# Optimization experiments

Hardware: AMD Instinct MI355X
Metric: run time of the kernel (lower is better)

## Reference

```python
import jax, jax.numpy as jnp
import numpy as np


def channel_linear(h, W, b):
    # h: (b, s, n_in, d_channels); W: (d, n_out, n_in); b: (d, n_out)
    out = jnp.einsum('bsic,coi->bsoc', h, W)
    return out + b.T[None, None]  # (b, s, n_out, d)


def setup_inputs() -> dict:
    d, s, bsz = 64, 64, 512
    lt, p = d * (d - 1) // 2, d * d
    key = jax.random.key(0)
    ks = jax.random.split(key, 12)
    inp = {
        'x': jax.random.normal(ks[0], (bsz, d), dtype=jnp.float32),
        'z': jax.random.normal(ks[1], (s, lt + p), dtype=jnp.float32),
    }
    widths = [d, 32, 32, 32, 1]
    for li, (ni, no) in enumerate(zip(widths[:-1], widths[1:])):
        inp[f'W{li}'] = jax.random.normal(ks[2 + 2 * li], (d, no, ni), dtype=jnp.float32) / np.sqrt(ni).astype(np.float32)
        inp[f'b{li}'] = jax.random.normal(ks[3 + 2 * li], (d, no), dtype=jnp.float32) * 0.01
    return inp


def reference(x, z, W0, b0, W1, b1, W2, b2, W3, b3):
    d = x.shape[1]
    s = z.shape[0]
    lt_width = d * (d - 1) // 2
    rows, cols = np.tril_indices(d, -1)  # matches torch.tril_indices(d, d, offset=-1)

    # get_z_adjacency_lt_p: strictly-lower-triangular matrix conjugated by z_p
    z_lt = jnp.zeros((s, d, d), dtype=z.dtype).at[:, rows, cols].set(z[:, :lt_width])
    z_p = z[:, -d * d:].reshape(s, d, d)
    # z_p^T @ z_lt @ z_p
    z_adj = jnp.einsum('sri,srt,stj->sij', z_p, z_lt, z_p)  # (s, d, d)

    # broadcast multiply: h[b,s,i,j] = A[s,i,j] * x[b,i]
    h = z_adj[None, :, :, :] * x[:, None, :, None]  # (b, s, d, d)

    h = jax.nn.relu(channel_linear(h, W0, b0))  # (b, s, 32, d)
    h = jax.nn.relu(channel_linear(h, W1, b1))
    h = jax.nn.relu(channel_linear(h, W2, b2))
    out = jnp.squeeze(channel_linear(h, W3, b3), axis=-2)  # (b, s, d)
    return (out, z_adj)
```

## Files before the change

kernel.cpp:

```cpp
#include <hip/hip_runtime.h>
#include <math.h>

#define D 64
#define S 64
#define BSZ 512
#define LTW 2016
#define ZROW 6112
#define OUT0_SIZE (BSZ * S * D)
#define ZADJ_OFF  OUT0_SIZE

typedef float    f32x4 __attribute__((ext_vector_type(4)));
typedef _Float16 f16x8 __attribute__((ext_vector_type(8)));
typedef _Float16 f16x2 __attribute__((ext_vector_type(2)));

union V8 { f16x8 v; f16x2 h2[4]; uint4 u; };

__device__ __forceinline__ f16x2 pkrtz(float a, float b) {
    return __builtin_bit_cast(f16x2, __builtin_amdgcn_cvt_pkrtz(a, b));
}

__global__ __launch_bounds__(256) void k_zadjprep(
    const float* __restrict__ z, float* __restrict__ zadj,
    float* __restrict__ zt,
    const float* __restrict__ x,
    const float* __restrict__ W0, const float* __restrict__ W1,
    const float* __restrict__ W2,
    uint4* __restrict__ w0f, uint4* __restrict__ w1f,
    uint4* __restrict__ w2f, uint4* __restrict__ xf) {
    __shared__ float zp[4096];
    __shared__ float zlt[4160];
    __shared__ float T[1280];
    const int blk = blockIdx.x;
    const int tid = threadIdx.x;

    if (blk < 256) {
        const int s = blk >> 2, jt = blk & 3;
        const float* zs = z + (size_t)s * ZROW;
#pragma unroll
        for (int rep = 0; rep < 16; ++rep) {
            int idx = tid + rep * 256;
            zp[idx] = zs[LTW + idx];
        }
        for (int idx = tid; idx < 4160; idx += 256) zlt[idx] = 0.0f;
        __syncthreads();
        for (int k = tid; k < LTW; k += 256) {
            float kf = (float)k;
            int r = (int)((1.0f + sqrtf(1.0f + 8.0f * kf)) * 0.5f);
            while (r * (r - 1) / 2 > k) --r;
            while ((r + 1) * r / 2 <= k) ++r;
            int t = k - r * (r - 1) / 2;
            zlt[r * 65 + t] = zs[k];
        }
        __syncthreads();
        const int rr = tid & 63, wj = (tid >> 6) * 4;
        {
            f32x4 acc = {0.0f, 0.0f, 0.0f, 0.0f};
            for (int t = 0; t < 64; ++t) {
                float zl = zlt[rr * 65 + t];
                f32x4 zpv = *(const f32x4*)&zp[t * 64 + jt * 16 + wj];
#pragma unroll
                for (int q = 0; q < 4; ++q) acc[q] = fmaf(zl, zpv[q], acc[q]);
            }
            *(f32x4*)&T[rr * 20 + wj] = acc;
        }
        __syncthreads();
        {
            const int i = rr;
            f32x4 acc = {0.0f, 0.0f, 0.0f, 0.0f};
            for (int r = 0; r < 64; ++r) {
                float zv = zp[r * 64 + i];
                f32x4 tv = *(const f32x4*)&T[r * 20 + wj];
#pragma unroll
                for (int q = 0; q < 4; ++q) acc[q] = fmaf(zv, tv[q], acc[q]);
            }
            *(f32x4*)&zadj[(size_t)s * 4096 + i * 64 + jt * 16 + wj] = acc;
            if (zt) {
#pragma unroll
                for (int q = 0; q < 4; ++q)
                    zt[(size_t)s * 4096 + (jt * 16 + wj + q) * 64 + i] = acc[q];
            }
        }
    } else {
        const int c = blk - 256;
        const int sl = tid >> 6, ln = tid & 63;
        const int q = ln >> 4, l15 = ln & 15;
        {
            int Mt = sl >> 1, ks = sl & 1;
            const float* src = W0 + c * 2048 + (Mt * 16 + l15) * 64 + ks * 32 + q * 8;
            V8 hv;
#pragma unroll
            for (int j = 0; j < 8; ++j) hv.v[j] = (_Float16)src[j];
            w0f[(size_t)(c * 4 + sl) * 64 + ln] = hv.u;
        }
        {
            const float* Wsrc = (sl < 2) ? W1 : W2;
            uint4* dstb = (sl < 2) ? w1f : w2f;
            int Mt = sl & 1;
            const float* srow = Wsrc + c * 1024 + (Mt * 16 + l15) * 32;
            V8 hv;
#pragma unroll
            for (int j = 0; j < 8; ++j) {
                int k = ((j >> 2) << 4) + q * 4 + (j & 3);
                hv.v[j] = (_Float16)srow[k];
            }
            dstb[(size_t)(c * 2 + Mt) * 64 + ln] = hv.u;
        }
        if (tid < 64) {
            int f = c * 64 + tid;
            int fln = f & 63, ks = (f >> 6) & 1, bt = f >> 7;
            int n = bt * 16 + (fln & 15), i0 = ks * 32 + (fln >> 4) * 8;
            const float* src = x + n * 64 + i0;
            V8 hv;
#pragma unroll
            for (int j = 0; j < 8; ++j) hv.v[j] = (_Float16)src[j];
            xf[f] = hv.u;
        }
    }
}

template <bool ZT>
__global__ __launch_bounds__(256, 4) void k_main_mfma(
    const uint4* __restrict__ xf, const uint4* __restrict__ w0f,
    const uint4* __restrict__ w1f, const uint4* __restrict__ w2f,
    const float* __restrict__ zadj, const float* __restrict__ zadjT,
    const float* __restrict__ B0, const float* __restrict__ B1,
    const float* __restrict__ B2, const float* __restrict__ W3,
    const float* __restrict__ B3, float* __restrict__ outT) {
    const int bh = blockIdx.x;
    const int c = blockIdx.y, sg = blockIdx.z;
    const int tid = threadIdx.x;
    const int wave = tid >> 6, lane = tid & 63;
    const int quad = lane >> 4;
    const int btbase = bh * 16 + wave * 4;

    V8 a0[2][2];
#pragma unroll
    for (int Mt = 0; Mt < 2; ++Mt)
#pragma unroll
        for (int ks = 0; ks < 2; ++ks)
            a0[Mt][ks].u = w0f[(size_t)(c * 4 + Mt * 2 + ks) * 64 + lane];
    V8 a1[2], a2[2];
#pragma unroll
    for (int Mt = 0; Mt < 2; ++Mt) {
        a1[Mt].u = w1f[(size_t)(c * 2 + Mt) * 64 + lane];
        a2[Mt].u = w2f[(size_t)(c * 2 + Mt) * 64 + lane];
    }
    f32x4 b0v[2], b1v[2], b2v[2], w3v[2];
#pragma unroll
    for (int Mt = 0; Mt < 2; ++Mt) {
        int off = c * 32 + Mt * 16 + quad * 4;
        b0v[Mt] = *(const f32x4*)(B0 + off);
        b1v[Mt] = *(const f32x4*)(B1 + off);
        b2v[Mt] = *(const f32x4*)(B2 + off);
        w3v[Mt] = *(const f32x4*)(W3 + off);
    }
    const float b3v = B3[c];

#pragma unroll 1
    for (int it = 0; it < 4; ++it) {
        const int s = sg * 4 + it;
        f16x2 zvh[2][4];
        if (ZT) {
            const f32x4* ztp = (const f32x4*)(zadjT + (size_t)s * 4096 + c * 64);
            f32x4 zq[4];
            zq[0] = ztp[quad * 2];
            zq[1] = ztp[quad * 2 + 1];
            zq[2] = ztp[8 + quad * 2];
            zq[3] = ztp[8 + quad * 2 + 1];
#pragma unroll
            for (int ks = 0; ks < 2; ++ks)
#pragma unroll
                for (int t = 0; t < 4; ++t) {
                    const f32x4& v = zq[ks * 2 + (t >> 1)];
                    zvh[ks][t] = pkrtz(v[(t & 1) * 2], v[(t & 1) * 2 + 1]);
                }
        } else {
#pragma unroll
            for (int ks = 0; ks < 2; ++ks) {
                const float* zp = zadj + (size_t)s * 4096 + (ks * 32 + quad * 8) * 64 + c;
                float zv[8];
#pragma unroll
                for (int j = 0; j < 8; ++j) zv[j] = zp[j * 64];
#pragma unroll
                for (int t = 0; t < 4; ++t)
                    zvh[ks][t] = pkrtz(zv[2 * t], zv[2 * t + 1]);
            }
        }
        V8 a0s[2][2];
#pragma unroll
        for (int Mt = 0; Mt < 2; ++Mt)
#pragma unroll
            for (int ks = 0; ks < 2; ++ks)
#pragma unroll
                for (int t = 0; t < 4; ++t)
                    a0s[Mt][ks].h2[t] = a0[Mt][ks].h2[t] * zvh[ks][t];

        float red[4];
#pragma unroll
        for (int Nt = 0; Nt < 4; ++Nt) {
            f32x4 acc0[2] = {b0v[0], b0v[1]};
#pragma unroll
            for (int ks = 0; ks < 2; ++ks) {
                V8 xv;
                xv.u = xf[(size_t)((btbase + Nt) * 2 + ks) * 64 + lane];
#pragma unroll
                for (int Mt = 0; Mt < 2; ++Mt)
                    acc0[Mt] = __builtin_amdgcn_mfma_f32_16x16x32_f16(
                        a0s[Mt][ks].v, xv.v, acc0[Mt], 0, 0, 0);
            }
            V8 bb;
            bb.h2[0] = pkrtz(fmaxf(acc0[0][0], 0.0f), fmaxf(acc0[0][1], 0.0f));
            bb.h2[1] = pkrtz(fmaxf(acc0[0][2], 0.0f), fmaxf(acc0[0][3], 0.0f));
            bb.h2[2] = pkrtz(fmaxf(acc0[1][0], 0.0f), fmaxf(acc0[1][1], 0.0f));
            bb.h2[3] = pkrtz(fmaxf(acc0[1][2], 0.0f), fmaxf(acc0[1][3], 0.0f));
            f32x4 acc1[2] = {b1v[0], b1v[1]};
#pragma unroll
            for (int Mt = 0; Mt < 2; ++Mt)
                acc1[Mt] = __builtin_amdgcn_mfma_f32_16x16x32_f16(
                    a1[Mt].v, bb.v, acc1[Mt], 0, 0, 0);
            V8 cc;
            cc.h2[0] = pkrtz(fmaxf(acc1[0][0], 0.0f), fmaxf(acc1[0][1], 0.0f));
            cc.h2[1] = pkrtz(fmaxf(acc1[0][2], 0.0f), fmaxf(acc1[0][3], 0.0f));
            cc.h2[2] = pkrtz(fmaxf(acc1[1][0], 0.0f), fmaxf(acc1[1][1], 0.0f));
            cc.h2[3] = pkrtz(fmaxf(acc1[1][2], 0.0f), fmaxf(acc1[1][3], 0.0f));
            f32x4 acc2[2] = {b2v[0], b2v[1]};
#pragma unroll
            for (int Mt = 0; Mt < 2; ++Mt)
                acc2[Mt] = __builtin_amdgcn_mfma_f32_16x16x32_f16(
                    a2[Mt].v, cc.v, acc2[Mt], 0, 0, 0);
            float p = 0.0f;
#pragma unroll
            for (int Mt = 0; Mt < 2; ++Mt)
#pragma unroll
                for (int r = 0; r < 4; ++r)
                    p = fmaf(w3v[Mt][r], fmaxf(acc2[Mt][r], 0.0f), p);
            p += __shfl_xor(p, 16, 64);
            p += __shfl_xor(p, 32, 64);
            red[Nt] = p;
        }
        float outv = (quad & 2) ? ((quad & 1) ? red[3] : red[2])
                                : ((quad & 1) ? red[1] : red[0]);
        outv += b3v;
        outT[((size_t)s * 64 + c) * 512 + bh * 256 + tid] = outv;
    }
}

__global__ __launch_bounds__(256, 3) void k_main_valu(
    const float* __restrict__ xsrc, const float* __restrict__ zadj,
    const float* __restrict__ W0, const float* __restrict__ B0,
    const float* __restrict__ W1, const float* __restrict__ B1,
    const float* __restrict__ W2, const float* __restrict__ B2,
    const float* __restrict__ W3, const float* __restrict__ B3,
    float* __restrict__ outp, int o_sS, int o_cS, int o_bS) {
    const int c = blockIdx.x;
    const int s = blockIdx.y;
    const int lane = threadIdx.x & 63;
    const int wave = threadIdx.x >> 6;

    const float* w0c = W0 + c * 2048;
    const float* w1c = W1 + c * 1024;
    const float* w2c = W2 + c * 1024;
    const float* w3c = W3 + c * 32;
    const float* b0c = B0 + c * 32;
    const float* b1c = B1 + c * 32;
    const float* b2c = B2 + c * 32;
    const float b3v = B3[c];
    const float* zc = zadj + s * 4096 + c;

#pragma unroll 1
    for (int bc = 0; bc < 2; ++bc) {
        const int b = wave * 128 + bc * 64 + lane;
        float h1[32], h2[32];
#pragma unroll
        for (int o = 0; o < 32; ++o) h1[o] = b0c[o];
#pragma unroll 8
        for (int i = 0; i < 64; ++i) {
            float hi = zc[i * 64] * xsrc[b * 64 + i];
#pragma unroll
            for (int o = 0; o < 32; ++o) h1[o] = fmaf(w0c[o * 64 + i], hi, h1[o]);
        }
#pragma unroll
        for (int o = 0; o < 32; ++o) { h1[o] = fmaxf(h1[o], 0.0f); h2[o] = b1c[o]; }
#pragma unroll 8
        for (int j = 0; j < 32; ++j) {
            float v = h1[j];
#pragma unroll
            for (int o = 0; o < 32; ++o) h2[o] = fmaf(w1c[o * 32 + j], v, h2[o]);
        }
#pragma unroll
        for (int o = 0; o < 32; ++o) { h2[o] = fmaxf(h2[o], 0.0f); h1[o] = b2c[o]; }
#pragma unroll 8
        for (int j = 0; j < 32; ++j) {
            float v = h2[j];
#pragma unroll
            for (int o = 0; o < 32; ++o) h1[o] = fmaf(w2c[o * 32 + j], v, h1[o]);
        }
        float a = b3v;
#pragma unroll
        for (int j = 0; j < 32; ++j) a = fmaf(w3c[j], fmaxf(h1[j], 0.0f), a);
        outp[s * o_sS + c * o_cS + b * o_bS] = a;
    }
}

__global__ __launch_bounds__(256) void k_outT(const float* __restrict__ outT,
                                              float* __restrict__ out) {
    __shared__ float tile[64][65];
    const int bt = blockIdx.x;
    const int s = blockIdx.y;
    const int tid = threadIdx.x;
    const int r0 = tid >> 6, q = tid & 63;
#pragma unroll
    for (int rep = 0; rep < 16; ++rep) {
        int crow = rep * 4 + r0;
        tile[crow][q] = outT[(s * 64 + crow) * 512 + bt * 64 + q];
    }
    __syncthreads();
#pragma unroll
    for (int rep = 0; rep < 16; ++rep) {
        int brow = rep * 4 + r0;
        out[(bt * 64 + brow) * 4096 + s * 64 + q] = tile[q][brow];
    }
}

extern "C" void kernel_launch(void* const* d_in, const int* in_sizes, int n_in,
                              void* d_out, int out_size, void* d_ws, size_t ws_size,
                              hipStream_t stream) {
    const float* x  = (const float*)d_in[0];
    const float* z  = (const float*)d_in[1];
    const float* W0 = (const float*)d_in[2];
    const float* B0 = (const float*)d_in[3];
    const float* W1 = (const float*)d_in[4];
    const float* B1 = (const float*)d_in[5];
    const float* W2 = (const float*)d_in[6];
    const float* B2 = (const float*)d_in[7];
    const float* W3 = (const float*)d_in[8];
    const float* B3 = (const float*)d_in[9];

    float* out  = (float*)d_out;
    float* zadj = out + ZADJ_OFF;

    const size_t OT_B  = (size_t)S * D * BSZ * sizeof(float);
    const size_t XF_B  = 4096 * 16;
    const size_t W0F_B = (size_t)64 * 4 * 64 * 16;
    const size_t W1F_B = (size_t)64 * 2 * 64 * 16;
    const size_t W2F_B = W1F_B;
    const size_t ZT_B  = (size_t)S * 4096 * sizeof(float);
    const size_t FRAG_END = OT_B + XF_B + W0F_B + W1F_B + W2F_B;
    const bool has_oT   = ws_size >= OT_B;
    const bool has_frag = ws_size >= FRAG_END;
    const bool has_zt   = ws_size >= FRAG_END + ZT_B;

    char* wsb = (char*)d_ws;
    float* outT  = (float*)wsb;
    uint4* xf    = (uint4*)(wsb + OT_B);
    uint4* w0f   = (uint4*)(wsb + OT_B + XF_B);
    uint4* w1f   = (uint4*)(wsb + OT_B + XF_B + W0F_B);
    uint4* w2f   = (uint4*)(wsb + OT_B + XF_B + W0F_B + W1F_B);
    float* zadjT = (float*)(wsb + FRAG_END);

    if (has_frag) {
        hipLaunchKernelGGL(k_zadjprep, dim3(320), dim3(256), 0, stream,
                           z, zadj, has_zt ? zadjT : (float*)nullptr,
                           x, W0, W1, W2, w0f, w1f, w2f, xf);
        if (has_zt)
            hipLaunchKernelGGL((k_main_mfma<true>), dim3(2, 64, 16), dim3(256),
                               0, stream, xf, w0f, w1f, w2f, zadj, zadjT,
                               B0, B1, B2, W3, B3, outT);
        else
            hipLaunchKernelGGL((k_main_mfma<false>), dim3(2, 64, 16), dim3(256),
                               0, stream, xf, w0f, w1f, w2f, zadj, zadjT,
                               B0, B1, B2, W3, B3, outT);
        hipLaunchKernelGGL(k_outT, dim3(8, S), dim3(256), 0, stream, outT, out);
    } else {
        hipLaunchKernelGGL(k_zadjprep, dim3(256), dim3(256), 0, stream,
                           z, zadj, (float*)nullptr, x, W0, W1, W2,
                           (uint4*)nullptr, (uint4*)nullptr, (uint4*)nullptr,
                           (uint4*)nullptr);
        float* op = has_oT ? outT : out;
        const int o_sS = has_oT ? (64 * 512) : 64;
        const int o_cS = has_oT ? 512 : 1;
        const int o_bS = has_oT ? 1 : 4096;
        hipLaunchKernelGGL(k_main_valu, dim3(D, S), dim3(256), 0, stream,
                           x, zadj, W0, B0, W1, B1, W2, B2, W3, B3,
                           op, o_sS, o_cS, o_bS);
        if (has_oT)
            hipLaunchKernelGGL(k_outT, dim3(8, S), dim3(256), 0, stream, outT, out);
    }
}
```

Measured before the change: 114.3 us.

## Hoist x fragments, apply packed fp16 ReLU, vectorize transpose, unroll prep loops

The x MFMA fragments are now loaded once into registers before the s-loop instead of being reloaded every iteration. ReLU is applied to the packed fp16 vectors after conversion rather than per float, and the launch bound drops to 3 waves per SIMD to leave room for the extra registers. The output transpose kernel switches to 16-byte vector global loads and stores, and the z-adjacency prep loops get unroll pragmas. The risks are lower occupancy, and that f16 ReLU after rounding-toward-zero conversion could differ slightly, though the results should be equivalent.

```diff
diff --git a/kernel.cpp b/kernel.cpp
--- a/kernel.cpp
+++ b/kernel.cpp
@@ -17,6 +17,16 @@
 
 __device__ __forceinline__ f16x2 pkrtz(float a, float b) {
     return __builtin_bit_cast(f16x2, __builtin_amdgcn_cvt_pkrtz(a, b));
+}
+__device__ __forceinline__ f16x8 relu8(f16x8 a) {
+#if __has_builtin(__builtin_elementwise_max)
+    return __builtin_elementwise_max(a, (f16x8)0);
+#else
+    f16x8 r;
+#pragma unroll
+    for (int i = 0; i < 8; ++i) r[i] = a[i] > (_Float16)0 ? a[i] : (_Float16)0;
+    return r;
+#endif
 }
 
 __global__ __launch_bounds__(256) void k_zadjprep(
@@ -55,6 +65,7 @@
         const int rr = tid & 63, wj = (tid >> 6) * 4;
         {
             f32x4 acc = {0.0f, 0.0f, 0.0f, 0.0f};
+#pragma unroll 8
             for (int t = 0; t < 64; ++t) {
                 float zl = zlt[rr * 65 + t];
                 f32x4 zpv = *(const f32x4*)&zp[t * 64 + jt * 16 + wj];
@@ -67,6 +78,7 @@
         {
             const int i = rr;
             f32x4 acc = {0.0f, 0.0f, 0.0f, 0.0f};
+#pragma unroll 8
             for (int r = 0; r < 64; ++r) {
                 float zv = zp[r * 64 + i];
                 f32x4 tv = *(const f32x4*)&T[r * 20 + wj];
@@ -119,7 +131,7 @@
 }
 
 template <bool ZT>
-__global__ __launch_bounds__(256, 4) void k_main_mfma(
+__global__ __launch_bounds__(256, 3) void k_main_mfma(
     const uint4* __restrict__ xf, const uint4* __restrict__ w0f,
     const uint4* __restrict__ w1f, const uint4* __restrict__ w2f,
     const float* __restrict__ zadj, const float* __restrict__ zadjT,
@@ -145,6 +157,12 @@
         a1[Mt].u = w1f[(size_t)(c * 2 + Mt) * 64 + lane];
         a2[Mt].u = w2f[(size_t)(c * 2 + Mt) * 64 + lane];
     }
+    V8 xv[4][2];
+#pragma unroll
+    for (int Nt = 0; Nt < 4; ++Nt)
+#pragma unroll
+        for (int ks = 0; ks < 2; ++ks)
+            xv[Nt][ks].u = xf[(size_t)((btbase + Nt) * 2 + ks) * 64 + lane];
     f32x4 b0v[2], b1v[2], b2v[2], w3v[2];
 #pragma unroll
     for (int Mt = 0; Mt < 2; ++Mt) {
@@ -200,29 +218,28 @@
         for (int Nt = 0; Nt < 4; ++Nt) {
             f32x4 acc0[2] = {b0v[0], b0v[1]};
 #pragma unroll
-            for (int ks = 0; ks < 2; ++ks) {
-                V8 xv;
-                xv.u = xf[(size_t)((btbase + Nt) * 2 + ks) * 64 + lane];
+            for (int ks = 0; ks < 2; ++ks)
 #pragma unroll
                 for (int Mt = 0; Mt < 2; ++Mt)
                     acc0[Mt] = __builtin_amdgcn_mfma_f32_16x16x32_f16(
-                        a0s[Mt][ks].v, xv.v, acc0[Mt], 0, 0, 0);
-            }
+                        a0s[Mt][ks].v, xv[Nt][ks].v, acc0[Mt], 0, 0, 0);
             V8 bb;
-            bb.h2[0] = pkrtz(fmaxf(acc0[0][0], 0.0f), fmaxf(acc0[0][1], 0.0f));
-            bb.h2[1] = pkrtz(fmaxf(acc0[0][2], 0.0f), fmaxf(acc0[0][3], 0.0f));
-            bb.h2[2] = pkrtz(fmaxf(acc0[1][0], 0.0f), fmaxf(acc0[1][1], 0.0f));
-            bb.h2[3] = pkrtz(fmaxf(acc0[1][2], 0.0f), fmaxf(acc0[1][3], 0.0f));
+            bb.h2[0] = pkrtz(acc0[0][0], acc0[0][1]);
+            bb.h2[1] = pkrtz(acc0[0][2], acc0[0][3]);
+            bb.h2[2] = pkrtz(acc0[1][0], acc0[1][1]);
+            bb.h2[3] = pkrtz(acc0[1][2], acc0[1][3]);
+            bb.v = relu8(bb.v);
             f32x4 acc1[2] = {b1v[0], b1v[1]};
 #pragma unroll
             for (int Mt = 0; Mt < 2; ++Mt)
                 acc1[Mt] = __builtin_amdgcn_mfma_f32_16x16x32_f16(
                     a1[Mt].v, bb.v, acc1[Mt], 0, 0, 0);
             V8 cc;
-            cc.h2[0] = pkrtz(fmaxf(acc1[0][0], 0.0f), fmaxf(acc1[0][1], 0.0f));
-            cc.h2[1] = pkrtz(fmaxf(acc1[0][2], 0.0f), fmaxf(acc1[0][3], 0.0f));
-            cc.h2[2] = pkrtz(fmaxf(acc1[1][0], 0.0f), fmaxf(acc1[1][1], 0.0f));
-            cc.h2[3] = pkrtz(fmaxf(acc1[1][2], 0.0f), fmaxf(acc1[1][3], 0.0f));
+            cc.h2[0] = pkrtz(acc1[0][0], acc1[0][1]);
+            cc.h2[1] = pkrtz(acc1[0][2], acc1[0][3]);
+            cc.h2[2] = pkrtz(acc1[1][0], acc1[1][1]);
+            cc.h2[3] = pkrtz(acc1[1][2], acc1[1][3]);
+            cc.v = relu8(cc.v);
             f32x4 acc2[2] = {b2v[0], b2v[1]};
 #pragma unroll
             for (int Mt = 0; Mt < 2; ++Mt)
@@ -304,21 +321,26 @@
 
 __global__ __launch_bounds__(256) void k_outT(const float* __restrict__ outT,
                                               float* __restrict__ out) {
-    __shared__ float tile[64][65];
+    __shared__ float tile[64 * 65];
     const int bt = blockIdx.x;
     const int s = blockIdx.y;
     const int tid = threadIdx.x;
-    const int r0 = tid >> 6, q = tid & 63;
-#pragma unroll
-    for (int rep = 0; rep < 16; ++rep) {
-        int crow = rep * 4 + r0;
-        tile[crow][q] = outT[(s * 64 + crow) * 512 + bt * 64 + q];
+    const int r16 = tid >> 4, q4 = (tid & 15) * 4;
+#pragma unroll
+    for (int rep = 0; rep < 4; ++rep) {
+        int crow = rep * 16 + r16;
+        f32x4 v = *(const f32x4*)&outT[(s * 64 + crow) * 512 + bt * 64 + q4];
+#pragma unroll
+        for (int i = 0; i < 4; ++i) tile[crow * 65 + q4 + i] = v[i];
     }
     __syncthreads();
 #pragma unroll
-    for (int rep = 0; rep < 16; ++rep) {
-        int brow = rep * 4 + r0;
-        out[(bt * 64 + brow) * 4096 + s * 64 + q] = tile[q][brow];
+    for (int rep = 0; rep < 4; ++rep) {
+        int brow = rep * 16 + r16;
+        f32x4 v;
+#pragma unroll
+        for (int i = 0; i < 4; ++i) v[i] = tile[(q4 + i) * 65 + brow];
+        *(f32x4*)&out[(bt * 64 + brow) * 4096 + s * 64 + q4] = v;
     }
 }
 
```

New measurement: 109.6 us. 1.04x faster.
